# Performance work log

Hardware: AMD Instinct MI355X
Metric: run time of the kernel (lower is better)

## Reference

```python
import jax, jax.numpy as jnp
import numpy as np

EXPAND = 2
KCONV = 4


def _mamba(x, Win, Wconv, bconv, Wx, Wdt, bdt, Alog, Dskip, Wout):
    # x: (B, C, H, W) -> flatten HW to a sequence, run Mamba (S6) block, reshape back
    B, C, H, W = x.shape
    L = H * W
    Di, Kc = Wconv.shape
    R = Wdt.shape[0]
    N = Alog.shape[1]
    xl = x.reshape(B, C, L).transpose(0, 2, 1)            # (B, L, C)
    xz = xl @ Win                                          # (B, L, 2*Di)
    xs, z = xz[..., :Di], xz[..., Di:]
    xt = xs.transpose(0, 2, 1)                             # (B, Di, L)
    xp = jnp.pad(xt, ((0, 0), (0, 0), (Kc - 1, 0)))        # causal depthwise conv1d
    conv = bconv[None, :, None]
    for k in range(Kc):
        conv = conv + Wconv[:, k][None, :, None] * xp[:, :, k:k + L]
    u = jax.nn.silu(conv).transpose(0, 2, 1)               # (B, L, Di)
    dbc = u @ Wx                                           # (B, L, R+2N)
    dt = jax.nn.softplus(dbc[..., :R] @ Wdt + bdt)         # (B, L, Di)
    Bm = dbc[..., R:R + N]                                 # (B, L, N)
    Cm = dbc[..., R + N:]                                  # (B, L, N)
    A = -jnp.exp(Alog)                                     # (Di, N)
    dA = jnp.exp(dt[..., None] * A)                        # (B, L, Di, N)
    dBx = dt[..., None] * Bm[:, :, None, :] * u[..., None] # (B, L, Di, N)

    def step(h, inp):
        a, bx, c = inp
        h = a * h + bx
        return h, jnp.einsum('bdn,bn->bd', h, c)

    h0 = jnp.zeros((B, Di, N), x.dtype)
    _, ys = jax.lax.scan(step, h0, (jnp.swapaxes(dA, 0, 1), jnp.swapaxes(dBx, 0, 1), jnp.swapaxes(Cm, 0, 1)))
    y = jnp.swapaxes(ys, 0, 1) + u * Dskip                 # (B, L, Di)
    y = y * jax.nn.silu(z)
    return (y @ Wout).transpose(0, 2, 1).reshape(B, C, H, W)


def _resize_bilinear(x, oh, ow):
    # F.interpolate(mode='bilinear', align_corners=True)
    B, C, H, W = x.shape
    ys = jnp.linspace(0.0, H - 1.0, oh)
    xs = jnp.linspace(0.0, W - 1.0, ow)
    y0 = jnp.floor(ys).astype(jnp.int32); y1 = jnp.clip(y0 + 1, 0, H - 1); wy = (ys - y0)[:, None]
    x0 = jnp.floor(xs).astype(jnp.int32); x1 = jnp.clip(x0 + 1, 0, W - 1); wx = (xs - x0)[None, :]
    r0 = x[:, :, y0, :]
    r1 = x[:, :, y1, :]
    top = r0[..., x0] * (1 - wx) + r0[..., x1] * wx
    bot = r1[..., x0] * (1 - wx) + r1[..., x1] * wx
    return top * (1 - wy) + bot * wy


def _mamba_params(key, D, N):
    Di = EXPAND * D
    R = max(1, D // 16)
    ks = jax.random.split(key, 6)
    s = 0.02
    Win = s * jax.random.normal(ks[0], (D, 2 * Di), jnp.float32)
    Wconv = s * jax.random.normal(ks[1], (Di, KCONV), jnp.float32)
    bconv = jnp.zeros((Di,), jnp.float32)
    Wx = s * jax.random.normal(ks[2], (Di, R + 2 * N), jnp.float32)
    Wdt = s * jax.random.normal(ks[3], (R, Di), jnp.float32)
    bdt = s * jax.random.normal(ks[4], (Di,), jnp.float32)
    Alog = jnp.tile(jnp.log(jnp.arange(1, N + 1, dtype=jnp.float32))[None, :], (Di, 1))
    Dskip = jnp.ones((Di,), jnp.float32)
    Wout = s * jax.random.normal(ks[5], (Di, D), jnp.float32)
    return Win, Wconv, bconv, Wx, Wdt, bdt, Alog, Dskip, Wout


def setup_inputs() -> dict:
    key = jax.random.key(0)
    C, B, N = 64, 2, 16
    sizes = [48, 24, 12, 6]
    ks = jax.random.split(key, 16)
    inp = {}
    for i, s in enumerate(sizes):
        inp[f'feat{i}'] = jax.random.normal(ks[i], (B, C, s, s), jnp.float32)
    names = ['Win', 'Wconv', 'bconv', 'Wx', 'Wdt', 'bdt', 'Alog', 'D', 'Wout']
    lvl = [_mamba_params(ks[4 + i], C, N) for i in range(4)]
    for j, nm in enumerate(names):
        inp['lvl_' + nm] = jnp.stack([lvl[i][j] for i in range(4)])
    cr = _mamba_params(ks[8], 4 * C, N)
    for j, nm in enumerate(names):
        inp['cr_' + nm] = cr[j]
    inp['proj_W'] = 0.02 * jax.random.normal(ks[9], (C, 4 * C), jnp.float32)  # 1x1 conv weight (out,in)
    inp['proj_b'] = jnp.zeros((C,), jnp.float32)
    inp['bn_g'] = jnp.ones((C,), jnp.float32)
    inp['bn_b'] = jnp.zeros((C,), jnp.float32)
    inp['bn_m'] = 0.1 * jax.random.normal(ks[10], (C,), jnp.float32)
    inp['bn_v'] = jax.random.uniform(ks[11], (C,), jnp.float32, minval=0.5, maxval=1.5)
    inp['target_h'] = 48
    inp['target_w'] = 48
    return inp


def reference(feat0, feat1, feat2, feat3,
              lvl_Win, lvl_Wconv, lvl_bconv, lvl_Wx, lvl_Wdt, lvl_bdt, lvl_Alog, lvl_D, lvl_Wout,
              cr_Win, cr_Wconv, cr_bconv, cr_Wx, cr_Wdt, cr_bdt, cr_Alog, cr_D, cr_Wout,
              proj_W, proj_b, bn_g, bn_b, bn_m, bn_v, target_h, target_w):
    feats = [feat0, feat1, feat2, feat3]
    processed = []
    for i, f in enumerate(feats):
        f = f + _mamba(f, lvl_Win[i], lvl_Wconv[i], lvl_bconv[i], lvl_Wx[i], lvl_Wdt[i],
                       lvl_bdt[i], lvl_Alog[i], lvl_D[i], lvl_Wout[i])
        processed.append(_resize_bilinear(f, target_h, target_w))
    x = jnp.concatenate(processed, axis=1)                 # (B, 4C, th, tw)
    x = x + _mamba(x, cr_Win, cr_Wconv, cr_bconv, cr_Wx, cr_Wdt, cr_bdt, cr_Alog, cr_D, cr_Wout)
    y = jnp.einsum('bchw,oc->bohw', x, proj_W) + proj_b[None, :, None, None]
    scale = (bn_g / jnp.sqrt(bn_v + 1e-5))[None, :, None, None]
    y = (y - bn_m[None, :, None, None]) * scale + bn_b[None, :, None, None]
    return jax.nn.relu(y)
```

## Files before the change

### kernel.cpp

```cpp
#include <hip/hip_runtime.h>
#include <cmath>

#define DEV __device__ __forceinline__

typedef unsigned short u16;
typedef u16 u16x8 __attribute__((ext_vector_type(8)));
typedef u16 u16x4 __attribute__((ext_vector_type(4)));
typedef short bf16x8 __attribute__((ext_vector_type(8)));
typedef float f32x4 __attribute__((ext_vector_type(4)));

constexpr int B_ = 2;
constexpr int S4[4]    = {48, 24, 12, 6};
constexpr int L4[4]    = {2304, 576, 144, 36};
constexpr int LOFF4[4] = {0, 2304, 2880, 3024};
constexpr int LTOT = 3060;
constexpr int TOFF4[4] = {0, 144, 180, 189};
constexpr int NTT = 192;
constexpr int NCH4[4]   = {36, 9, 3, 1};
constexpr int CHOFF4[4] = {0, 36, 45, 48};
constexpr int NCHL = 49;
constexpr int NCHC = 36;
constexpr int LC = 2304;
constexpr float LOG2E = 1.44269504088896f;

DEV float siluf(float x) { return x / (1.f + __expf(-x)); }
DEV float softplusf(float x) { return fmaxf(x, 0.f) + log1pf(__expf(-fabsf(x))); }
DEV float b2f(u16 x) { union { float f; unsigned u; } v; v.u = ((unsigned)x) << 16; return v.f; }
DEV u16 f2b(float f) {
  union { float f; unsigned u; } v; v.f = f;
  unsigned r = v.u + 0x7fffu + ((v.u >> 16) & 1u);
  return (u16)(r >> 16);
}

__global__ __launch_bounds__(256) void k_prep(
    const float* __restrict__ projW, const float* __restrict__ crWout,
    const float* __restrict__ cWin, const float* __restrict__ cWx,
    float* __restrict__ Wt, float* __restrict__ WP,
    u16* __restrict__ WinT, float* __restrict__ WxT) {
  __shared__ float sm[64 * 65];
  int blk = blockIdx.x;
  int tid = threadIdx.x;
  if (blk < 64) {
    int i = blk * 256 + tid;
    int o = i >> 8, c = i & 255;
    Wt[c * 64 + o] = projW[o * 256 + c];
  } else if (blk < 192) {
    int i = (blk - 64) * 256 + tid;
    int d = i >> 6, o = i & 63;
    float acc = 0.f;
#pragma unroll 4
    for (int c = 0; c < 256; ++c)
      acc = fmaf(crWout[d * 256 + c], projW[o * 256 + c], acc);
    WP[d * 64 + o] = acc;
  } else if (blk < 256) {
    int t = blk - 192;
    int ct = t & 3, nt = t >> 2;
    int c0 = ct * 64, n0 = nt * 64;
    for (int i = tid; i < 4096; i += 256) {
      int cc = i >> 6, nn = i & 63;
      sm[cc * 65 + nn] = cWin[(size_t)(c0 + cc) * 1024 + n0 + nn];
    }
    __syncthreads();
    for (int i = tid; i < 4096; i += 256) {
      int nn = i >> 6, cc = i & 63;
      WinT[(size_t)(n0 + nn) * 256 + c0 + cc] = f2b(sm[cc * 65 + nn]);
    }
  } else {
    int i = (blk - 256) * 256 + tid;
    int d = i & 511, j = i >> 9;
    WxT[j * 512 + d] = cWx[d * 48 + j];
  }
}

__global__ __launch_bounds__(256) void k_front_lvl(
    const float* __restrict__ f0, const float* __restrict__ f1,
    const float* __restrict__ f2, const float* __restrict__ f3,
    const float* __restrict__ Win,
    const float* __restrict__ Wconv,
    const float* __restrict__ bconv,
    const float* __restrict__ Wx,
    const float* __restrict__ Wdt,
    const float* __restrict__ bdt,
    u16* __restrict__ u_l, u16* __restrict__ dt_l,
    u16* __restrict__ Bm_l, u16* __restrict__ Cm_l, u16* __restrict__ z_l) {
  __shared__ float s_x[64 * 20];
  __shared__ float s_xs[19 * 128];
  __shared__ float s_u[16 * 132];
  __shared__ float s_dbc[16 * 36];
  int bid = blockIdx.x;
  int b = bid / NTT, t = bid - b * NTT;
  int lvl = 0;
  while (lvl < 3 && t >= TOFF4[lvl + 1]) ++lvl;
  int tl = t - TOFF4[lvl];
  int L = L4[lvl], loff = LOFF4[lvl];
  int l0 = tl * 16;
  int nl = min(16, L - l0);
  const float* fx = lvl == 0 ? f0 : lvl == 1 ? f1 : lvl == 2 ? f2 : f3;
  int tid = threadIdx.x;

  for (int i = tid; i < 64 * 20; i += 256) {
    int c = i / 20, r = i - c * 20;
    int l = l0 - 3 + r;
    float v = 0.f;
    if (r < 19 && l >= 0 && l < L) v = fx[(size_t)(b * 64 + c) * L + l];
    s_x[i] = v;
  }
  __syncthreads();
  {
    int j = tid;
    float acc[19];
#pragma unroll
    for (int r = 0; r < 19; ++r) acc[r] = 0.f;
    const float* W = Win + lvl * 64 * 256 + j;
    for (int c = 0; c < 64; ++c) {
      float w = W[c * 256];
#pragma unroll
      for (int r = 0; r < 19; ++r) acc[r] = fmaf(w, s_x[c * 20 + r], acc[r]);
    }
    if (j < 128) {
#pragma unroll
      for (int r = 0; r < 19; ++r) s_xs[r * 128 + j] = acc[r];
    } else {
      int d = j - 128;
      int dti = d >> 4, jj = d & 15;
      for (int r = 3; r < 19; ++r) {
        int l = l0 - 3 + r;
        if (l < l0 + nl)
          z_l[((size_t)(b * 8 + dti) * LTOT + loff + l) * 16 + jj] = f2b(acc[r]);
      }
    }
  }
  __syncthreads();
  for (int i = tid; i < 16 * 128; i += 256) {
    int l = i >> 7, d = i & 127;
    if (l < nl) {
      const float* wc = Wconv + (lvl * 128 + d) * 4;
      float a = bconv[lvl * 128 + d];
#pragma unroll
      for (int k = 0; k < 4; ++k) a = fmaf(wc[k], s_xs[(l + k) * 128 + d], a);
      float uu = siluf(a);
      s_u[l * 132 + d] = uu;
      u_l[((size_t)(b * 8 + (d >> 4)) * LTOT + loff + l0 + l) * 16 + (d & 15)] = f2b(uu);
    }
  }
  __syncthreads();
  for (int i = tid; i < 16 * 36; i += 256) {
    int l = i & 15, jj = i >> 4;
    if (l < nl) {
      const float* wx = Wx + lvl * 128 * 36 + jj;
      float a = 0.f;
      for (int d = 0; d < 128; ++d) a = fmaf(s_u[l * 132 + d], wx[d * 36], a);
      s_dbc[l * 36 + jj] = a;
      if (jj >= 4) {
        int q = jj - 4;
        size_t gb = ((size_t)(b * LTOT) + loff + l0 + l) * 16;
        if (q < 16) Bm_l[gb + q] = f2b(a);
        else        Cm_l[gb + (q - 16)] = f2b(a);
      }
    }
  }
  __syncthreads();
  for (int i = tid; i < 16 * 128; i += 256) {
    int l = i >> 7, d = i & 127;
    if (l < nl) {
      float a = bdt[lvl * 128 + d];
#pragma unroll
      for (int r = 0; r < 4; ++r)
        a = fmaf(s_dbc[l * 36 + r], Wdt[(lvl * 4 + r) * 128 + d], a);
      dt_l[((size_t)(b * 8 + (d >> 4)) * LTOT + loff + l0 + l) * 16 + (d & 15)] =
          f2b(softplusf(a));
    }
  }
}

template <int MODE, int PASSC>
__global__ __launch_bounds__(256) void k_scan(
    const u16* __restrict__ dtb, const u16* __restrict__ ub,
    const u16* __restrict__ Bmb, const u16* __restrict__ Cmb,
    const u16* __restrict__ zb,
    const float* __restrict__ Alog, const float* __restrict__ Dsk,
    float* __restrict__ hloc, float* __restrict__ Ssum,
    const float* __restrict__ hin, u16* __restrict__ yg) {
  constexpr int DI = MODE ? 512 : 128;
  constexpr int NDT = DI / 16;
  constexpr int NCHT = MODE ? NCHC : NCHL;
  constexpr int LT = MODE ? LC : LTOT;
  constexpr int NARR = PASSC ? 5 : 3;
  __shared__ __align__(16) u16 smem[NARR * 1024];
  u16* s_dt = smem;
  u16* s_u = smem + 1024;
  u16* s_B = smem + 2048;
  u16* s_C = PASSC ? smem + 3072 : nullptr;
  u16* s_y = PASSC ? smem + 4096 : nullptr;

  int bid = blockIdx.x;
  int dti = bid % NDT;
  int rem = bid / NDT;
  int gc = rem % NCHT;
  int b = rem / NCHT;
  int lvl = 0, ch = gc, Lq = LC, loff = 0;
  if (MODE == 0) {
    while (lvl < 3 && gc >= CHOFF4[lvl + 1]) ++lvl;
    ch = gc - CHOFF4[lvl];
    Lq = L4[lvl];
    loff = LOFF4[lvl];
  }
  int l0 = ch * 64;
  int len = min(64, Lq - l0);
  int labs0 = loff + l0;
  int tid = threadIdx.x;
  int n = tid & 15, dd = tid >> 4;
  int d = dti * 16 + dd;

  size_t base2 = ((size_t)(b * NDT + dti) * LT + labs0) * 16;
  size_t baseB = ((size_t)b * LT + labs0) * 16;
  {
    int nv = len * 2;
    const u16x8* pdt = (const u16x8*)(dtb + base2);
    const u16x8* pu  = (const u16x8*)(ub + base2);
    const u16x8* pB  = (const u16x8*)(Bmb + baseB);
    u16x8* qdt = (u16x8*)s_dt;
    u16x8* qu  = (u16x8*)s_u;
    u16x8* qB  = (u16x8*)s_B;
    for (int i = tid; i < nv; i += 256) {
      qdt[i] = pdt[i];
      qu[i]  = pu[i];
      qB[i]  = pB[i];
    }
    if (PASSC) {
      const u16x8* pC = (const u16x8*)(Cmb + baseB);
      u16x8* qC = (u16x8*)s_C;
      for (int i = tid; i < nv; i += 256) qC[i] = pC[i];
    }
  }
  __syncthreads();

  int ai = (MODE ? d : lvl * 128 + d);
  float kA2 = -__expf(Alog[ai * 16 + n]) * LOG2E;
  size_t hix = (((size_t)(b * NCHT) + gc) * DI + d) * 16 + n;
  float h = 0.f, ss = 0.f;
  if (PASSC) h = hin[hix];
  float dsk = PASSC ? Dsk[ai] : 0.f;

#pragma unroll 2
  for (int l = 0; l < len; ++l) {
    float dt = b2f(s_dt[l * 16 + dd]);
    float uu = b2f(s_u[l * 16 + dd]);
    float bm = b2f(s_B[l * 16 + n]);
    float dA = exp2f(kA2 * dt);
    h = fmaf(dA, h, dt * uu * bm);
    if (PASSC) {
      float p = h * b2f(s_C[l * 16 + n]);
      p += __shfl_xor(p, 1, 16);
      p += __shfl_xor(p, 2, 16);
      p += __shfl_xor(p, 4, 16);
      p += __shfl_xor(p, 8, 16);
      if (n == 0) s_y[l * 16 + dd] = f2b(fmaf(uu, dsk, p));
    } else {
      ss += dt;
    }
  }
  if (!PASSC) {
    hloc[hix] = h;
    if (n == 0) Ssum[((size_t)(b * NCHT) + gc) * DI + d] = ss;
  } else {
    __syncthreads();
    for (int i = tid; i < len * 16; i += 256) {
      float z = b2f(zb[base2 + i]);
      float gate = z / (1.f + __expf(-z));
      yg[base2 + i] = f2b(b2f(s_y[i]) * gate);
    }
  }
}

__global__ __launch_bounds__(256) void k_combine_lvl(
    const float* __restrict__ Alog, const float* __restrict__ hloc,
    const float* __restrict__ Ssum, float* __restrict__ hin) {
  int i = blockIdx.x * 256 + threadIdx.x;
  int n = i & 15, d = (i >> 4) & 127, lvl = (i >> 11) & 3, b = i >> 13;
  float kA2 = -__expf(Alog[(lvl * 128 + d) * 16 + n]) * LOG2E;
  float h = 0.f;
  int nch = NCH4[lvl];
  for (int ch = 0; ch < nch; ++ch) {
    int gc = CHOFF4[lvl] + ch;
    size_t ix = (((size_t)(b * NCHL) + gc) * 128 + d) * 16 + n;
    hin[ix] = h;
    float S = Ssum[((size_t)(b * NCHL) + gc) * 128 + d];
    h = fmaf(exp2f(kA2 * S), h, hloc[ix]);
  }
}

__global__ __launch_bounds__(256) void k_combine_cr(
    const float* __restrict__ Alog, const float* __restrict__ hloc,
    const float* __restrict__ Ssum, float* __restrict__ hin) {
  int i = blockIdx.x * 256 + threadIdx.x;
  int n = i & 15, d = (i >> 4) & 511, b = i >> 13;
  float kA2 = -__expf(Alog[d * 16 + n]) * LOG2E;
  float h = 0.f;
  for (int ch = 0; ch < NCHC; ++ch) {
    size_t ix = (((size_t)(b * NCHC) + ch) * 512 + d) * 16 + n;
    hin[ix] = h;
    float S = Ssum[((size_t)(b * NCHC) + ch) * 512 + d];
    h = fmaf(exp2f(kA2 * S), h, hloc[ix]);
  }
}

__global__ __launch_bounds__(256) void k_out_lvl(
    const u16* __restrict__ yg_l, const float* __restrict__ Wout,
    const float* __restrict__ f0, const float* __restrict__ f1,
    const float* __restrict__ f2, const float* __restrict__ f3,
    float* __restrict__ fout) {
  __shared__ float s_ygT[128 * 20];
  __shared__ float s_o[16 * 64];
  int bid = blockIdx.x;
  int b = bid / NTT, t = bid - b * NTT;
  int lvl = 0;
  while (lvl < 3 && t >= TOFF4[lvl + 1]) ++lvl;
  int tl = t - TOFF4[lvl];
  int L = L4[lvl], loff = LOFF4[lvl];
  int l0 = tl * 16, nl = min(16, L - l0);
  const float* fx = lvl == 0 ? f0 : lvl == 1 ? f1 : lvl == 2 ? f2 : f3;
  int tid = threadIdx.x;
  for (int i = tid; i < 16 * 128; i += 256) {
    int d = i & 127, l = i >> 7;
    float v = 0.f;
    if (l < nl)
      v = b2f(yg_l[((size_t)(b * 8 + (d >> 4)) * LTOT + loff + l0 + l) * 16 + (d & 15)]);
    s_ygT[d * 20 + l] = v;
  }
  __syncthreads();
  {
    int c = tid & 63, lg = (tid >> 6) * 4;
    float acc[4] = {0.f, 0.f, 0.f, 0.f};
    const float* W = Wout + lvl * 128 * 64 + c;
    for (int dq = 0; dq < 128; ++dq) {
      float w = W[dq * 64];
      float4 yv = *(const float4*)&s_ygT[dq * 20 + lg];
      acc[0] = fmaf(w, yv.x, acc[0]);
      acc[1] = fmaf(w, yv.y, acc[1]);
      acc[2] = fmaf(w, yv.z, acc[2]);
      acc[3] = fmaf(w, yv.w, acc[3]);
    }
#pragma unroll
    for (int a = 0; a < 4; ++a) s_o[(lg + a) * 64 + c] = acc[a];
  }
  __syncthreads();
  for (int i = tid; i < 16 * 64; i += 256) {
    int c = i >> 4, l = i & 15;
    if (l < nl)
      fout[((size_t)(b * 64) + c) * LTOT + loff + l0 + l] =
          s_o[l * 64 + c] + fx[((size_t)(b * 64) + c) * L + l0 + l];
  }
}

__global__ __launch_bounds__(256) void k_resize(const float* __restrict__ fout,
                                                float* __restrict__ xTf,
                                                u16* __restrict__ xTb) {
  int i = blockIdx.x * 256 + threadIdx.x;
  int ch = i & 255;
  int rem = i >> 8;
  int hw = rem % 2304;
  int b = rem / 2304;
  int oh = hw / 48, ow = hw - oh * 48;
  int lvl = ch >> 6, c = ch & 63;
  int s = S4[lvl];
  const float* base = fout + ((size_t)(b * 64) + c) * LTOT + LOFF4[lvl];
  float scl = (float)(s - 1) * (1.f / 47.f);
  float fy = oh * scl, fxx = ow * scl;
  int y0 = (int)floorf(fy), x0 = (int)floorf(fxx);
  float wy = fy - y0, wx = fxx - x0;
  int y1 = min(y0 + 1, s - 1), x1 = min(x0 + 1, s - 1);
  float v00 = base[y0 * s + x0], v01 = base[y0 * s + x1];
  float v10 = base[y1 * s + x0], v11 = base[y1 * s + x1];
  float top = v00 * (1.f - wx) + v01 * wx;
  float bot = v10 * (1.f - wx) + v11 * wx;
  float v = top * (1.f - wy) + bot * wy;
  xTf[i] = v;
  xTb[i] = f2b(v);
}

__global__ __launch_bounds__(256) void k_gemm_mfma(
    const u16* __restrict__ xT,
    const u16* __restrict__ WT,
    u16* __restrict__ xs_c, u16* __restrict__ z_c) {
  __shared__ __align__(16) u16 s_a[64 * 72];
  __shared__ __align__(16) u16 s_b[128 * 72];
  int bid = blockIdx.x;
  int nj = bid & 7, bm = bid >> 3;
  int tid = threadIdx.x;
  int lane = tid & 63, w = tid >> 6;
  int wm = (w & 1) * 32, wn = (w >> 1) * 64;
  const int m_base = bm * 64;
  const int n_base = nj * 128;

  f32x4 acc[2][4];
#pragma unroll
  for (int mi = 0; mi < 2; ++mi)
#pragma unroll
    for (int ni = 0; ni < 4; ++ni) acc[mi][ni] = {0.f, 0.f, 0.f, 0.f};

  u16x8 ra0, ra1, rb0, rb1, rb2, rb3;
  auto ld = [&](int c0) {
#pragma unroll
    for (int s = 0; s < 2; ++s) {
      int v = s * 256 + tid;
      int row = v >> 3, kc = (v & 7) * 8;
      u16x8 t = *(const u16x8*)&xT[(size_t)(m_base + row) * 256 + c0 + kc];
      if (s == 0) ra0 = t; else ra1 = t;
    }
#pragma unroll
    for (int s = 0; s < 4; ++s) {
      int v = s * 256 + tid;
      int row = v >> 3, kc = (v & 7) * 8;
      u16x8 t = *(const u16x8*)&WT[(size_t)(n_base + row) * 256 + c0 + kc];
      if (s == 0) rb0 = t; else if (s == 1) rb1 = t;
      else if (s == 2) rb2 = t; else rb3 = t;
    }
  };
  auto st = [&]() {
#pragma unroll
    for (int s = 0; s < 2; ++s) {
      int v = s * 256 + tid;
      int row = v >> 3, kc = (v & 7) * 8;
      *(u16x8*)&s_a[row * 72 + kc] = (s == 0) ? ra0 : ra1;
    }
#pragma unroll
    for (int s = 0; s < 4; ++s) {
      int v = s * 256 + tid;
      int row = v >> 3, kc = (v & 7) * 8;
      const u16x8& t = (s == 0) ? rb0 : (s == 1) ? rb1 : (s == 2) ? rb2 : rb3;
      *(u16x8*)&s_b[row * 72 + kc] = t;
    }
  };
  ld(0);
  int mlane = lane & 15, kg = (lane >> 4) * 8;
  for (int kt = 0; kt < 4; ++kt) {
    st();
    __syncthreads();
    if (kt < 3) ld((kt + 1) * 64);
#pragma unroll
    for (int kk = 0; kk < 2; ++kk) {
      int k0 = kk * 32 + kg;
      bf16x8 af[2], bfr[4];
#pragma unroll
      for (int mi = 0; mi < 2; ++mi)
        af[mi] = *(const bf16x8*)&s_a[(wm + mi * 16 + mlane) * 72 + k0];
#pragma unroll
      for (int ni = 0; ni < 4; ++ni)
        bfr[ni] = *(const bf16x8*)&s_b[(wn + ni * 16 + mlane) * 72 + k0];
#pragma unroll
      for (int mi = 0; mi < 2; ++mi)
#pragma unroll
        for (int ni = 0; ni < 4; ++ni)
          acc[mi][ni] = __builtin_amdgcn_mfma_f32_16x16x32_bf16(
              af[mi], bfr[ni], acc[mi][ni], 0, 0, 0);
    }
    __syncthreads();
  }
  int rgrp = (lane >> 4) * 4;
#pragma unroll
  for (int mi = 0; mi < 2; ++mi) {
#pragma unroll
    for (int ni = 0; ni < 4; ++ni) {
      int n = n_base + wn + ni * 16 + mlane;
#pragma unroll
      for (int r = 0; r < 4; ++r) {
        int gm = m_base + wm + mi * 16 + rgrp + r;
        int b = gm >= 2304;
        int l = gm - b * 2304;
        u16 v = f2b(acc[mi][ni][r]);
        if (n < 512) {
          xs_c[((size_t)(b * LC) + l) * 512 + n] = v;
        } else {
          int dz = n - 512;
          z_c[((size_t)(b * 32 + (dz >> 4)) * LC + l) * 16 + (dz & 15)] = v;
        }
      }
    }
  }
}

__global__ __launch_bounds__(256) void k_mid_cr(
    const u16* __restrict__ xs_c,
    const float* __restrict__ Wconv,
    const float* __restrict__ bconv,
    const float* __restrict__ WxT,
    const float* __restrict__ Wdt,
    const float* __restrict__ bdt, u16* __restrict__ u_c,
    u16* __restrict__ dt_c, u16* __restrict__ Bm_c, u16* __restrict__ Cm_c) {
  __shared__ __align__(16) u16 s_xs[11 * 512];
  __shared__ __align__(16) float s_u[8 * 516];
  __shared__ float s_dbc[8 * 48];
  int bid = blockIdx.x;
  int b = bid / 288, tl = bid - b * 288;
  int l0 = tl * 8;
  int tid = threadIdx.x;
  for (int i = tid; i < 704; i += 256) {
    int r = i >> 6;
    int l = l0 - 3 + r;
    u16x8 v = {0, 0, 0, 0, 0, 0, 0, 0};
    if (l >= 0)
      v = *(const u16x8*)&xs_c[((size_t)(b * LC) + l) * 512 + (i & 63) * 8];
    *(u16x8*)&s_xs[i * 8] = v;
  }
  __syncthreads();
  for (int i = tid; i < 8 * 512; i += 256) {
    int l = i >> 9, d = i & 511;
    const float* wc = Wconv + d * 4;
    float a = bconv[d];
#pragma unroll
    for (int k = 0; k < 4; ++k) a = fmaf(wc[k], b2f(s_xs[(l + k) * 512 + d]), a);
    float uu = siluf(a);
    s_u[l * 516 + d] = uu;
    u_c[((size_t)(b * 32 + (d >> 4)) * LC + l0 + l) * 16 + (d & 15)] = f2b(uu);
  }
  __syncthreads();
  for (int i = tid; i < 8 * 48; i += 256) {
    int jj = i >> 3, l = i & 7;
    const float* wx = WxT + jj * 512;
    float a = 0.f;
#pragma unroll 4
    for (int d = 0; d < 512; d += 4) {
      float4 w4 = *(const float4*)&wx[d];
      float4 u4 = *(const float4*)&s_u[l * 516 + d];
      a = fmaf(w4.x, u4.x, a);
      a = fmaf(w4.y, u4.y, a);
      a = fmaf(w4.z, u4.z, a);
      a = fmaf(w4.w, u4.w, a);
    }
    s_dbc[l * 48 + jj] = a;
    if (jj >= 16) {
      int q = jj - 16;
      size_t gb = ((size_t)(b * LC) + l0 + l) * 16;
      if (q < 16) Bm_c[gb + q] = f2b(a);
      else        Cm_c[gb + (q - 16)] = f2b(a);
    }
  }
  __syncthreads();
  for (int i = tid; i < 8 * 512; i += 256) {
    int l = i >> 9, d = i & 511;
    float a = bdt[d];
#pragma unroll
    for (int r = 0; r < 16; ++r)
      a = fmaf(s_dbc[l * 48 + r], Wdt[r * 512 + d], a);
    dt_c[((size_t)(b * 32 + (d >> 4)) * LC + l0 + l) * 16 + (d & 15)] =
        f2b(softplusf(a));
  }
}

__global__ __launch_bounds__(256) void k_final(
    const float* __restrict__ xTf, const u16* __restrict__ yg_c,
    const float* __restrict__ Wt, const float* __restrict__ WP,
    const float* __restrict__ pb, const float* __restrict__ bng,
    const float* __restrict__ bnb, const float* __restrict__ bnm,
    const float* __restrict__ bnv, float* __restrict__ out) {
  __shared__ float s_xc[256 * 8];
  __shared__ float s_yg[512 * 8];
  __shared__ float s_w[32 * 64];
  int bid = blockIdx.x;
  int b = bid / 288, tl = bid - b * 288;
  int l0 = tl * 8;
  int tid = threadIdx.x;
  for (int i = tid; i < 2048; i += 256) {
    int c = i & 255, l = i >> 8;
    s_xc[c * 8 + l] = xTf[((size_t)(b * 2304) + l0 + l) * 256 + c];
  }
  for (int i = tid; i < 4096; i += 256) {
    int j = i & 15, l = (i >> 4) & 7, dt = i >> 7;
    s_yg[(dt * 16 + j) * 8 + l] =
        b2f(yg_c[((size_t)(b * 32 + dt) * LC + l0 + l) * 16 + j]);
  }
  int o = tid & 63, lg = (tid >> 6) * 2;
  float acc0 = 0.f, acc1 = 0.f;
  float4 r0, r1;
  auto ldT = [&](const float* W, int kt, float4& a0, float4& a1) {
#pragma unroll
    for (int s = 0; s < 2; ++s) {
      int idx = s * 256 + tid;
      int row = idx >> 4, c4 = (idx & 15) << 2;
      float4 v = *(const float4*)&W[(kt * 32 + row) * 64 + c4];
      if (s == 0) a0 = v; else a1 = v;
    }
  };
  auto stT = [&](const float4& a0, const float4& a1) {
#pragma unroll
    for (int s = 0; s < 2; ++s) {
      int idx = s * 256 + tid;
      int row = idx >> 4, c4 = (idx & 15) << 2;
      *(float4*)&s_w[row * 64 + c4] = (s == 0) ? a0 : a1;
    }
  };
  ldT(Wt, 0, r0, r1);
  __syncthreads();
  stT(r0, r1);
  __syncthreads();
  for (int kt = 0; kt < 8; ++kt) {
    if (kt < 7) ldT(Wt, kt + 1, r0, r1);
    else ldT(WP, 0, r0, r1);
#pragma unroll
    for (int cc = 0; cc < 32; ++cc) {
      float w = s_w[cc * 64 + o];
      float2 xv = *(const float2*)&s_xc[(kt * 32 + cc) * 8 + lg];
      acc0 = fmaf(w, xv.x, acc0);
      acc1 = fmaf(w, xv.y, acc1);
    }
    __syncthreads();
    stT(r0, r1);
    __syncthreads();
  }
  for (int kt = 0; kt < 16; ++kt) {
    if (kt < 15) ldT(WP, kt + 1, r0, r1);
#pragma unroll
    for (int cc = 0; cc < 32; ++cc) {
      float w = s_w[cc * 64 + o];
      float2 yv = *(const float2*)&s_yg[(kt * 32 + cc) * 8 + lg];
      acc0 = fmaf(w, yv.x, acc0);
      acc1 = fmaf(w, yv.y, acc1);
    }
    __syncthreads();
    if (kt < 15) {
      stT(r0, r1);
      __syncthreads();
    }
  }
  float bias = pb[o], m = bnm[o], g = bng[o], v = bnv[o], bb = bnb[o];
  float scl = g * (1.f / sqrtf(v + 1e-5f));
  float2 r;
  r.x = fmaxf((acc0 + bias - m) * scl + bb, 0.f);
  r.y = fmaxf((acc1 + bias - m) * scl + bb, 0.f);
  *(float2*)&out[((size_t)(b * 64) + o) * LC + l0 + lg] = r;
}

extern "C" void kernel_launch(void* const* d_in, const int* in_sizes, int n_in,
                              void* d_out, int out_size, void* d_ws,
                              size_t ws_size, hipStream_t stream) {
  (void)in_sizes; (void)n_in; (void)out_size; (void)ws_size;
  const float* f0 = (const float*)d_in[0];
  const float* f1 = (const float*)d_in[1];
  const float* f2 = (const float*)d_in[2];
  const float* f3 = (const float*)d_in[3];
  const float* lWin   = (const float*)d_in[4];
  const float* lWconv = (const float*)d_in[5];
  const float* lbconv = (const float*)d_in[6];
  const float* lWx    = (const float*)d_in[7];
  const float* lWdt   = (const float*)d_in[8];
  const float* lbdt   = (const float*)d_in[9];
  const float* lAlog  = (const float*)d_in[10];
  const float* lD     = (const float*)d_in[11];
  const float* lWout  = (const float*)d_in[12];
  const float* cWin   = (const float*)d_in[13];
  const float* cWconv = (const float*)d_in[14];
  const float* cbconv = (const float*)d_in[15];
  const float* cWx    = (const float*)d_in[16];
  const float* cWdt   = (const float*)d_in[17];
  const float* cbdt   = (const float*)d_in[18];
  const float* cAlog  = (const float*)d_in[19];
  const float* cD     = (const float*)d_in[20];
  const float* cWout  = (const float*)d_in[21];
  const float* projW  = (const float*)d_in[22];
  const float* projb  = (const float*)d_in[23];
  const float* bng    = (const float*)d_in[24];
  const float* bnb    = (const float*)d_in[25];
  const float* bnm    = (const float*)d_in[26];
  const float* bnv    = (const float*)d_in[27];
  float* out = (float*)d_out;

  float* ws = (float*)d_ws;
  size_t off = 0;
  auto allocf = [&](size_t n) { float* p = ws + off; off += (n + 7) & ~(size_t)7; return p; };
  auto allocb = [&](size_t n) { u16* p = (u16*)(ws + off); off += ((n + 1) / 2 + 7) & ~(size_t)7; return p; };

  float* Wt     = allocf(256 * 64);
  float* WP     = allocf(512 * 64);
  float* WxT    = allocf(48 * 512);
  float* fout   = allocf((size_t)B_ * 64 * LTOT);
  float* xTf    = allocf((size_t)B_ * LC * 256);
  float* hloc_l = allocf((size_t)B_ * NCHL * 128 * 16);
  float* S_l    = allocf((size_t)B_ * NCHL * 128);
  float* hin_l  = allocf((size_t)B_ * NCHL * 128 * 16);
  float* hloc_c = allocf((size_t)B_ * NCHC * 512 * 16);
  float* S_c    = allocf((size_t)B_ * NCHC * 512);
  float* hin_c  = allocf((size_t)B_ * NCHC * 512 * 16);

  u16* WinT  = allocb(1024 * 256);
  u16* xTb   = allocb((size_t)B_ * LC * 256);
  u16* u_l2  = allocb((size_t)B_ * 8 * LTOT * 16);
  u16* dt_l2 = allocb((size_t)B_ * 8 * LTOT * 16);
  u16* z_l2  = allocb((size_t)B_ * 8 * LTOT * 16);
  u16* yg_l2 = allocb((size_t)B_ * 8 * LTOT * 16);
  u16* Bm_l2 = allocb((size_t)B_ * LTOT * 16);
  u16* Cm_l2 = allocb((size_t)B_ * LTOT * 16);
  u16* xs_c2 = allocb((size_t)B_ * LC * 512);
  u16* u_c2  = allocb((size_t)B_ * 32 * LC * 16);
  u16* dt_c2 = allocb((size_t)B_ * 32 * LC * 16);
  u16* z_c2  = allocb((size_t)B_ * 32 * LC * 16);
  u16* yg_c2 = allocb((size_t)B_ * 32 * LC * 16);
  u16* Bm_c2 = allocb((size_t)B_ * LC * 16);
  u16* Cm_c2 = allocb((size_t)B_ * LC * 16);

  k_prep<<<352, 256, 0, stream>>>(projW, cWout, cWin, cWx, Wt, WP, WinT, WxT);

  k_front_lvl<<<B_ * NTT, 256, 0, stream>>>(f0, f1, f2, f3, lWin, lWconv,
                                            lbconv, lWx, lWdt, lbdt, u_l2,
                                            dt_l2, Bm_l2, Cm_l2, z_l2);

  k_scan<0, 0><<<B_ * 8 * NCHL, 256, 0, stream>>>(
      dt_l2, u_l2, Bm_l2, Cm_l2, nullptr, lAlog, lD, hloc_l, S_l, nullptr,
      nullptr);
  k_combine_lvl<<<64, 256, 0, stream>>>(lAlog, hloc_l, S_l, hin_l);
  k_scan<0, 1><<<B_ * 8 * NCHL, 256, 0, stream>>>(
      dt_l2, u_l2, Bm_l2, Cm_l2, z_l2, lAlog, lD, nullptr, nullptr, hin_l,
      yg_l2);

  k_out_lvl<<<B_ * NTT, 256, 0, stream>>>(yg_l2, lWout, f0, f1, f2, f3, fout);
  k_resize<<<(B_ * 256 * LC) / 256, 256, 0, stream>>>(fout, xTf, xTb);

  k_gemm_mfma<<<72 * 8, 256, 0, stream>>>(xTb, WinT, xs_c2, z_c2);
  k_mid_cr<<<B_ * 288, 256, 0, stream>>>(xs_c2, cWconv, cbconv, WxT, cWdt,
                                         cbdt, u_c2, dt_c2, Bm_c2, Cm_c2);

  k_scan<1, 0><<<B_ * 32 * NCHC, 256, 0, stream>>>(
      dt_c2, u_c2, Bm_c2, Cm_c2, nullptr, cAlog, cD, hloc_c, S_c, nullptr,
      nullptr);
  k_combine_cr<<<64, 256, 0, stream>>>(cAlog, hloc_c, S_c, hin_c);
  k_scan<1, 1><<<B_ * 32 * NCHC, 256, 0, stream>>>(
      dt_c2, u_c2, Bm_c2, Cm_c2, z_c2, cAlog, cD, nullptr, nullptr, hin_c,
      yg_c2);

  k_final<<<B_ * 288, 256, 0, stream>>>(xTf, yg_c2, Wt, WP, projb, bng, bnb,
                                        bnm, bnv, out);
}
```

Before: 357.6 us.

## Give each scan thread four SSM states and cover 64 channels per block

The chunked selective-scan kernel now assigns four state elements per thread instead of one, so each block covers 64 channels (four 16-channel tiles) rather than 16. The shared B/C tiles are loaded once per block and reused across more channels. Each step needs two shuffles instead of four, and dt/u loads are amortised over four state updates. The gating epilogue is vectorised to 8-wide bf16. The cost is four times fewer blocks, which may reduce occupancy and parallelism, especially for the small per-level scan grids.

Result: faster. 350.6 us (-2.0%).

```diff
diff --git a/kernel.cpp b/kernel.cpp
--- a/kernel.cpp
+++ b/kernel.cpp
@@ -183,19 +183,19 @@
     const float* __restrict__ hin, u16* __restrict__ yg) {
   constexpr int DI = MODE ? 512 : 128;
   constexpr int NDT = DI / 16;
+  constexpr int NB = DI / 64;
   constexpr int NCHT = MODE ? NCHC : NCHL;
   constexpr int LT = MODE ? LC : LTOT;
-  constexpr int NARR = PASSC ? 5 : 3;
-  __shared__ __align__(16) u16 smem[NARR * 1024];
+  __shared__ __align__(16) u16 smem[PASSC ? 14336 : 9216];
   u16* s_dt = smem;
-  u16* s_u = smem + 1024;
-  u16* s_B = smem + 2048;
-  u16* s_C = PASSC ? smem + 3072 : nullptr;
-  u16* s_y = PASSC ? smem + 4096 : nullptr;
+  u16* s_u  = smem + 4096;
+  u16* s_B  = smem + 8192;
+  u16* s_C  = PASSC ? smem + 9216 : nullptr;
+  u16* s_y  = PASSC ? smem + 10240 : nullptr;
 
   int bid = blockIdx.x;
-  int dti = bid % NDT;
-  int rem = bid / NDT;
+  int dblk = bid % NB;
+  int rem = bid / NB;
   int gc = rem % NCHT;
   int b = rem / NCHT;
   int lvl = 0, ch = gc, Lq = LC, loff = 0;
@@ -209,66 +209,90 @@
   int len = min(64, Lq - l0);
   int labs0 = loff + l0;
   int tid = threadIdx.x;
-  int n = tid & 15, dd = tid >> 4;
-  int d = dti * 16 + dd;
-
-  size_t base2 = ((size_t)(b * NDT + dti) * LT + labs0) * 16;
-  size_t baseB = ((size_t)b * LT + labs0) * 16;
+  int q = tid & 3;
+  int dl = (tid >> 2) & 15;
+  int ti_l = tid >> 6;
+  int dti = dblk * 4 + ti_l;
+  int d = dti * 16 + dl;
+  int n0 = q * 4;
+
+  for (int ti = 0; ti < 4; ++ti) {
+    size_t g2 = ((size_t)(b * NDT + dblk * 4 + ti) * LT + labs0) * 16;
+    const u16x8* pdt = (const u16x8*)(dtb + g2);
+    const u16x8* pu  = (const u16x8*)(ub + g2);
+    for (int i = tid; i < len * 2; i += 256) {
+      *(u16x8*)&s_dt[ti * 1024 + i * 8] = pdt[i];
+      *(u16x8*)&s_u [ti * 1024 + i * 8] = pu[i];
+    }
+  }
   {
-    int nv = len * 2;
-    const u16x8* pdt = (const u16x8*)(dtb + base2);
-    const u16x8* pu  = (const u16x8*)(ub + base2);
-    const u16x8* pB  = (const u16x8*)(Bmb + baseB);
-    u16x8* qdt = (u16x8*)s_dt;
-    u16x8* qu  = (u16x8*)s_u;
-    u16x8* qB  = (u16x8*)s_B;
-    for (int i = tid; i < nv; i += 256) {
-      qdt[i] = pdt[i];
-      qu[i]  = pu[i];
-      qB[i]  = pB[i];
-    }
+    size_t gB = ((size_t)b * LT + labs0) * 16;
+    for (int i = tid; i < len * 2; i += 256) {
+      *(u16x8*)&s_B[i * 8] = *(const u16x8*)&Bmb[gB + i * 8];
+      if (PASSC) *(u16x8*)&s_C[i * 8] = *(const u16x8*)&Cmb[gB + i * 8];
+    }
+  }
+  __syncthreads();
+
+  int ai = (MODE ? d : lvl * 128 + d);
+  float4 al = *(const float4*)&Alog[ai * 16 + n0];
+  float kA2[4] = {-__expf(al.x) * LOG2E, -__expf(al.y) * LOG2E,
+                  -__expf(al.z) * LOG2E, -__expf(al.w) * LOG2E};
+  size_t hix = (((size_t)(b * NCHT) + gc) * DI + d) * 16 + n0;
+  float h[4] = {0.f, 0.f, 0.f, 0.f};
+  if (PASSC) {
+    float4 hv = *(const float4*)&hin[hix];
+    h[0] = hv.x; h[1] = hv.y; h[2] = hv.z; h[3] = hv.w;
+  }
+  float dsk = PASSC ? Dsk[ai] : 0.f;
+  float ss = 0.f;
+
+  for (int l = 0; l < len; ++l) {
+    float dt = b2f(s_dt[ti_l * 1024 + l * 16 + dl]);
+    float uu = b2f(s_u [ti_l * 1024 + l * 16 + dl]);
+    float dtu = dt * uu;
+    u16x4 Bv = *(const u16x4*)&s_B[l * 16 + n0];
     if (PASSC) {
-      const u16x8* pC = (const u16x8*)(Cmb + baseB);
-      u16x8* qC = (u16x8*)s_C;
-      for (int i = tid; i < nv; i += 256) qC[i] = pC[i];
-    }
-  }
-  __syncthreads();
-
-  int ai = (MODE ? d : lvl * 128 + d);
-  float kA2 = -__expf(Alog[ai * 16 + n]) * LOG2E;
-  size_t hix = (((size_t)(b * NCHT) + gc) * DI + d) * 16 + n;
-  float h = 0.f, ss = 0.f;
-  if (PASSC) h = hin[hix];
-  float dsk = PASSC ? Dsk[ai] : 0.f;
-
-#pragma unroll 2
-  for (int l = 0; l < len; ++l) {
-    float dt = b2f(s_dt[l * 16 + dd]);
-    float uu = b2f(s_u[l * 16 + dd]);
-    float bm = b2f(s_B[l * 16 + n]);
-    float dA = exp2f(kA2 * dt);
-    h = fmaf(dA, h, dt * uu * bm);
-    if (PASSC) {
-      float p = h * b2f(s_C[l * 16 + n]);
-      p += __shfl_xor(p, 1, 16);
-      p += __shfl_xor(p, 2, 16);
-      p += __shfl_xor(p, 4, 16);
-      p += __shfl_xor(p, 8, 16);
-      if (n == 0) s_y[l * 16 + dd] = f2b(fmaf(uu, dsk, p));
+      u16x4 Cv = *(const u16x4*)&s_C[l * 16 + n0];
+      float p = 0.f;
+#pragma unroll
+      for (int i = 0; i < 4; ++i) {
+        float dA = exp2f(kA2[i] * dt);
+        h[i] = fmaf(dA, h[i], dtu * b2f(Bv[i]));
+        p = fmaf(h[i], b2f(Cv[i]), p);
+      }
+      p += __shfl_xor(p, 1, 4);
+      p += __shfl_xor(p, 2, 4);
+      if (q == 0) s_y[l * 64 + ti_l * 16 + dl] = f2b(fmaf(uu, dsk, p));
     } else {
+#pragma unroll
+      for (int i = 0; i < 4; ++i) {
+        float dA = exp2f(kA2[i] * dt);
+        h[i] = fmaf(dA, h[i], dtu * b2f(Bv[i]));
+      }
       ss += dt;
     }
   }
   if (!PASSC) {
-    hloc[hix] = h;
-    if (n == 0) Ssum[((size_t)(b * NCHT) + gc) * DI + d] = ss;
+    f32x4 hv = {h[0], h[1], h[2], h[3]};
+    *(f32x4*)&hloc[hix] = hv;
+    if (q == 0) Ssum[((size_t)(b * NCHT) + gc) * DI + d] = ss;
   } else {
     __syncthreads();
-    for (int i = tid; i < len * 16; i += 256) {
-      float z = b2f(zb[base2 + i]);
-      float gate = z / (1.f + __expf(-z));
-      yg[base2 + i] = f2b(b2f(s_y[i]) * gate);
+    for (int ti = 0; ti < 4; ++ti) {
+      size_t g2 = ((size_t)(b * NDT + dblk * 4 + ti) * LT + labs0) * 16;
+      for (int i = tid; i < len * 2; i += 256) {
+        u16x8 zv = *(const u16x8*)&zb[g2 + i * 8];
+        u16x8 yv = *(const u16x8*)&s_y[(i >> 1) * 64 + ti * 16 + (i & 1) * 8];
+        u16x8 o;
+#pragma unroll
+        for (int j = 0; j < 8; ++j) {
+          float z = b2f(zv[j]);
+          float gate = z / (1.f + __expf(-z));
+          o[j] = f2b(b2f(yv[j]) * gate);
+        }
+        *(u16x8*)&yg[g2 + i * 8] = o;
+      }
     }
   }
 }
@@ -704,11 +728,11 @@
                                             lbconv, lWx, lWdt, lbdt, u_l2,
                                             dt_l2, Bm_l2, Cm_l2, z_l2);
 
-  k_scan<0, 0><<<B_ * 8 * NCHL, 256, 0, stream>>>(
+  k_scan<0, 0><<<B_ * NCHL * 2, 256, 0, stream>>>(
       dt_l2, u_l2, Bm_l2, Cm_l2, nullptr, lAlog, lD, hloc_l, S_l, nullptr,
       nullptr);
   k_combine_lvl<<<64, 256, 0, stream>>>(lAlog, hloc_l, S_l, hin_l);
-  k_scan<0, 1><<<B_ * 8 * NCHL, 256, 0, stream>>>(
+  k_scan<0, 1><<<B_ * NCHL * 2, 256, 0, stream>>>(
       dt_l2, u_l2, Bm_l2, Cm_l2, z_l2, lAlog, lD, nullptr, nullptr, hin_l,
       yg_l2);
 
@@ -719,11 +743,11 @@
   k_mid_cr<<<B_ * 288, 256, 0, stream>>>(xs_c2, cWconv, cbconv, WxT, cWdt,
                                          cbdt, u_c2, dt_c2, Bm_c2, Cm_c2);
 
-  k_scan<1, 0><<<B_ * 32 * NCHC, 256, 0, stream>>>(
+  k_scan<1, 0><<<B_ * NCHC * 8, 256, 0, stream>>>(
       dt_c2, u_c2, Bm_c2, Cm_c2, nullptr, cAlog, cD, hloc_c, S_c, nullptr,
       nullptr);
   k_combine_cr<<<64, 256, 0, stream>>>(cAlog, hloc_c, S_c, hin_c);
-  k_scan<1, 1><<<B_ * 32 * NCHC, 256, 0, stream>>>(
+  k_scan<1, 1><<<B_ * NCHC * 8, 256, 0, stream>>>(
       dt_c2, u_c2, Bm_c2, Cm_c2, z_c2, cAlog, cD, nullptr, nullptr, hin_c,
       yg_c2);
 
```
